# Kernel tuning notes

Hardware: AMD Instinct MI355X
Metric: run time of the kernel (lower is better)

## Reference

```python
import jax, jax.numpy as jnp
import numpy as np

B, N, IN_DIM, OUT_DIM, H = 8, 1024, 256, 256, 4
HD = OUT_DIM // H  # head_dim = 64
NEG = -1e9
EPS = 1e-5


def setup_inputs() -> dict:
    key = jax.random.key(0)
    ks = jax.random.split(key, 9)
    h = jax.random.normal(ks[0], (B, N, IN_DIM), dtype=jnp.float32)
    adj = jax.random.randint(ks[1], (N, N), 0, 2, dtype=jnp.int32)
    adj = adj.at[jnp.arange(N), jnp.arange(N)].set(1)  # self loops so no empty rows
    s = 1.0 / np.sqrt(IN_DIM)
    W = jax.random.uniform(ks[2], (H, IN_DIM, HD), jnp.float32, -s, s)
    sa = 1.0 / np.sqrt(2 * HD)
    a1 = jax.random.uniform(ks[3], (H, HD), jnp.float32, -sa, sa)
    a2 = jax.random.uniform(ks[4], (H, HD), jnp.float32, -sa, sa)
    sp = 1.0 / np.sqrt(OUT_DIM)
    proj_w = jax.random.uniform(ks[5], (OUT_DIM, OUT_DIM), jnp.float32, -sp, sp)
    proj_b = jax.random.uniform(ks[6], (OUT_DIM,), jnp.float32, -sp, sp)
    gamma = jnp.ones((OUT_DIM,), jnp.float32)
    beta = jnp.zeros((OUT_DIM,), jnp.float32)
    return {"h": h, "adj": adj, "W": W, "a1": a1, "a2": a2,
            "proj_w": proj_w, "proj_b": proj_b, "gamma": gamma, "beta": beta}


def reference(h, adj, W, a1, a2, proj_w, proj_b, gamma, beta):
    # Wh: [B,H,N,HD]
    Wh = jnp.einsum('bni,hid->bhnd', h, W)
    # Decompose a([Wh_i || Wh_j]) = a1.Wh_i + a2.Wh_j (same math as concat+linear)
    si = jnp.einsum('bhnd,hd->bhn', Wh, a1)  # [B,H,N]
    sj = jnp.einsum('bhnd,hd->bhn', Wh, a2)
    e = jax.nn.leaky_relu(si[:, :, :, None] + sj[:, :, None, :], 0.2)  # [B,H,N,N]
    mask = (adj == 0)  # [N,N]
    e = jnp.where(mask[None, None], NEG, e)
    alpha = jax.nn.softmax(e, axis=-1)
    out = jnp.einsum('bhnm,bhmd->bhnd', alpha, Wh)  # [B,H,N,HD]
    h_multi = out.transpose(0, 2, 1, 3).reshape(B, N, OUT_DIM)  # concat heads
    h_out = jnp.einsum('bnd,od->bno', h_multi, proj_w) + proj_b
    h_out = h_out + h  # residual (in_dim == out_dim)
    mu = jnp.mean(h_out, axis=-1, keepdims=True)
    var = jnp.mean(jnp.square(h_out - mu), axis=-1, keepdims=True)
    return (h_out - mu) * jax.lax.rsqrt(var + EPS) * gamma + beta
```

## Files before the change

### kernel.cpp

```cpp
#include <hip/hip_runtime.h>
#include <hip/hip_bf16.h>

#define NN 1024

typedef __attribute__((ext_vector_type(8))) short short8;
typedef __attribute__((ext_vector_type(4))) short short4e;
typedef __attribute__((ext_vector_type(4))) float floatx4;
typedef __attribute__((ext_vector_type(4))) int intx4;

static __device__ __forceinline__ short bfb(float x) {
    return (short)__bfloat16_as_ushort(__float2bfloat16(x));
}

__global__ __launch_bounds__(256) void prep_kernel(
    const float* __restrict__ W, const float* __restrict__ proj_w,
    const int* __restrict__ adj,
    __hip_bfloat16* __restrict__ WTb,
    __hip_bfloat16* __restrict__ pwb,
    unsigned* __restrict__ adjm)
{
    int blk = blockIdx.x, t = threadIdx.x;
    if (blk < 16) {
        int o = blk * 16 + (t >> 4);
        int hh = o >> 6, d = o & 63;
        #pragma unroll
        for (int kk = 0; kk < 16; ++kk) {
            int k = (t & 15) + 16 * kk;
            WTb[(size_t)o * 256 + k] = __float2bfloat16(W[((size_t)hh * 256 + k) * 64 + d]);
        }
    } else if (blk < 32) {
        size_t base = (size_t)(blk - 16) * 4096 + (size_t)t * 16;
        #pragma unroll
        for (int k = 0; k < 16; k += 4) {
            floatx4 v = *(const floatx4*)(proj_w + base + k);
            short4e tmp;
            #pragma unroll
            for (int j = 0; j < 4; ++j) tmp[j] = bfb(v[j]);
            *(short4e*)(pwb + base + k) = tmp;
        }
    } else {
        int n = (blk - 32) * 8 + (t >> 5);
        int wd = t & 31;
        const int* arow = adj + (size_t)n * NN + wd * 32;
        unsigned bits = 0;
        #pragma unroll
        for (int j4 = 0; j4 < 8; ++j4) {
            intx4 v = *(const intx4*)(arow + j4 * 4);
            #pragma unroll
            for (int j = 0; j < 4; ++j) if (v[j] != 0) bits |= (1u << (j4 * 4 + j));
        }
        adjm[(size_t)n * 32 + wd] = bits;
    }
}

__global__ __launch_bounds__(256) void wh_kernel(
    const float* __restrict__ h,
    const __hip_bfloat16* __restrict__ WTb,
    const float* __restrict__ a1, const float* __restrict__ a2,
    __hip_bfloat16* __restrict__ WhT,
    float* __restrict__ si, float* __restrict__ sj)
{
    int t = threadIdx.x;
    int w = t >> 6, l = t & 63;
    int rl = l & 15, q = l >> 4;
    int r0 = blockIdx.x * 16;
    int bb = r0 >> 10;
    int n0 = r0 & 1023;

    __shared__ float redsi[4][4][16];
    __shared__ float redsj[4][4][16];

    short8 af[8];
    const float* Arow = h + (size_t)(r0 + rl) * 256 + q * 8;
    #pragma unroll
    for (int k0 = 0; k0 < 8; ++k0) {
        floatx4 v0 = *(const floatx4*)(Arow + k0 * 32);
        floatx4 v1 = *(const floatx4*)(Arow + k0 * 32 + 4);
        short8 a;
        #pragma unroll
        for (int j = 0; j < 4; ++j) { a[j] = bfb(v0[j]); a[j + 4] = bfb(v1[j]); }
        af[k0] = a;
    }

    float a1v[4], a2v[4];
    #pragma unroll
    for (int j = 0; j < 4; ++j) {
        a1v[j] = a1[j * 64 + w * 16 + rl];
        a2v[j] = a2[j * 64 + w * 16 + rl];
    }

    short8 bcur[8];
    {
        const __hip_bfloat16* B0 = WTb + (size_t)(w * 16 + rl) * 256 + q * 8;
        #pragma unroll
        for (int k0 = 0; k0 < 8; ++k0) bcur[k0] = *(const short8*)(B0 + k0 * 32);
    }

    #pragma unroll
    for (int j = 0; j < 4; ++j) {
        short8 bnxt[8];
        if (j < 3) {
            const __hip_bfloat16* Bn = WTb + (size_t)((w + (j + 1) * 4) * 16 + rl) * 256 + q * 8;
            #pragma unroll
            for (int k0 = 0; k0 < 8; ++k0) bnxt[k0] = *(const short8*)(Bn + k0 * 32);
        }

        floatx4 acc = {0.f, 0.f, 0.f, 0.f};
        #pragma unroll
        for (int k0 = 0; k0 < 8; ++k0)
            acc = __builtin_amdgcn_mfma_f32_16x16x32_bf16(af[k0], bcur[k0], acc, 0, 0, 0);

        short4e tmp;
        #pragma unroll
        for (int i = 0; i < 4; ++i) tmp[i] = bfb(acc[i]);
        *(short4e*)(WhT + ((size_t)(bb * 4 + j) * 64 + w * 16 + rl) * NN + n0 + q * 4) = tmp;

        #pragma unroll
        for (int i = 0; i < 4; ++i) {
            float p1 = acc[i] * a1v[j];
            float p2 = acc[i] * a2v[j];
            #pragma unroll
            for (int off = 1; off < 16; off <<= 1) {
                p1 += __shfl_xor(p1, off, 64);
                p2 += __shfl_xor(p2, off, 64);
            }
            if (rl == 0) { redsi[w][j][q * 4 + i] = p1; redsj[w][j][q * 4 + i] = p2; }
        }

        #pragma unroll
        for (int z = 0; z < 8; ++z) bcur[z] = bnxt[z];
    }
    __syncthreads();

    if (w == 0) {
        int head = l >> 4, row = l & 15;
        float s = redsi[0][head][row] + redsi[1][head][row] + redsi[2][head][row] + redsi[3][head][row];
        si[(size_t)(bb * 4 + head) * NN + n0 + row] = s;
    } else if (w == 1) {
        int head = l >> 4, row = l & 15;
        float s = redsj[0][head][row] + redsj[1][head][row] + redsj[2][head][row] + redsj[3][head][row];
        sj[(size_t)(bb * 4 + head) * NN + n0 + row] = s;
    }
}

__global__ __launch_bounds__(256) void attn_proj_kernel(
    const unsigned* __restrict__ adjm,
    const __hip_bfloat16* __restrict__ WhT,
    const float* __restrict__ si, const float* __restrict__ sj,
    const __hip_bfloat16* __restrict__ pwb,
    const float* __restrict__ h,
    const float* __restrict__ proj_b, const float* __restrict__ gamma,
    const float* __restrict__ beta,
    float* __restrict__ out)
{
    int blk = blockIdx.x, t = threadIdx.x;
    int w = t >> 6, l = t & 63;
    int rl = l & 15, q = l >> 4;
    int b = blk >> 6, n0 = (blk & 63) * 16;
    int bh = b * 4 + w;
    int r0 = blk * 16;

    __shared__ __align__(16) __hip_bfloat16 p_lds[4][16 * 136];
    __shared__ __align__(16) __hip_bfloat16 hm_stage[16][264];
    __shared__ float rinvs[4][16];
    __shared__ float red[2][4][16];

    int r = l >> 2, cg = l & 3;
    float sii = si[(size_t)bh * NN + n0 + r];
    const float* sjr = sj + (size_t)bh * NN;
    const unsigned* amrow = adjm + (size_t)(n0 + r) * 32;

    __hip_bfloat16* pt = &p_lds[w][0];
    const __hip_bfloat16* Ab = pt + rl * 136 + q * 8;
    const __hip_bfloat16* Bbase = WhT + ((size_t)bh * 64 + rl) * NN + q * 8;

    float lsum = 0.f;
    floatx4 acc[4] = { {0,0,0,0}, {0,0,0,0}, {0,0,0,0}, {0,0,0,0} };

#define SCORE_BLOCK(ITX)                                                        \
    do {                                                                        \
        int mb_ = (ITX) * 128 + cg * 32;                                        \
        unsigned bits_ = amrow[mb_ >> 5];                                       \
        short8 pv_[4];                                                          \
        _Pragma("unroll")                                                       \
        for (int c4 = 0; c4 < 8; ++c4) {                                        \
            floatx4 s4_ = *(const floatx4*)(sjr + mb_ + c4 * 4);                \
            _Pragma("unroll")                                                   \
            for (int k = 0; k < 4; ++k) {                                       \
                float x_ = sii + s4_[k];                                        \
                x_ = x_ > 0.f ? x_ : 0.2f * x_;                                 \
                x_ = ((bits_ >> (c4 * 4 + k)) & 1u) ? x_ : -1e9f;               \
                float pv = __expf(x_);                                          \
                lsum += pv;                                                     \
                pv_[c4 >> 1][(c4 & 1) * 4 + k] = bfb(pv);                       \
            }                                                                   \
        }                                                                       \
        short8* dst_ = (short8*)(pt + r * 136 + cg * 32);                       \
        dst_[0] = pv_[0]; dst_[1] = pv_[1]; dst_[2] = pv_[2]; dst_[3] = pv_[3]; \
    } while (0)

    short8 bcur[16];
    #pragma unroll
    for (int ks = 0; ks < 4; ++ks)
        #pragma unroll
        for (int dt = 0; dt < 4; ++dt)
            bcur[ks * 4 + dt] = *(const short8*)(Bbase + (size_t)dt * 16 * NN + ks * 32);
    SCORE_BLOCK(0);

    #pragma unroll
    for (int it = 0; it < 8; ++it) {
        short8 bnxt[16];
        if (it < 7) {
            int m1 = (it + 1) * 128;
            #pragma unroll
            for (int ks = 0; ks < 4; ++ks)
                #pragma unroll
                for (int dt = 0; dt < 4; ++dt)
                    bnxt[ks * 4 + dt] = *(const short8*)(Bbase + (size_t)dt * 16 * NN + m1 + ks * 32);
        }
        #pragma unroll
        for (int ks = 0; ks < 4; ++ks) {
            short8 afr = *(const short8*)(Ab + ks * 32);
            #pragma unroll
            for (int dt = 0; dt < 4; ++dt)
                acc[dt] = __builtin_amdgcn_mfma_f32_16x16x32_bf16(afr, bcur[ks * 4 + dt], acc[dt], 0, 0, 0);
        }
        if (it < 7) {
            SCORE_BLOCK(it + 1);
            #pragma unroll
            for (int z = 0; z < 16; ++z) bcur[z] = bnxt[z];
        }
    }
#undef SCORE_BLOCK

    lsum += __shfl_xor(lsum, 1, 64);
    lsum += __shfl_xor(lsum, 2, 64);
    if (cg == 0) rinvs[w][r] = 1.f / lsum;
    float riv[4];
    #pragma unroll
    for (int i = 0; i < 4; ++i) riv[i] = rinvs[w][q * 4 + i];

    #pragma unroll
    for (int dt = 0; dt < 4; ++dt) {
        #pragma unroll
        for (int i = 0; i < 4; ++i)
            hm_stage[q * 4 + i][w * 64 + dt * 16 + rl] = __float2bfloat16(acc[dt][i] * riv[i]);
    }
    __syncthreads();

    short8 paf[8];
    const __hip_bfloat16* Arow2 = &hm_stage[rl][0] + q * 8;
    #pragma unroll
    for (int k0 = 0; k0 < 8; ++k0) paf[k0] = *(const short8*)(Arow2 + k0 * 32);

    floatx4 pacc[4];
    #pragma unroll
    for (int j = 0; j < 4; ++j) {
        int ct = w + j * 4;
        const __hip_bfloat16* Brow = pwb + (size_t)(ct * 16 + rl) * 256 + q * 8;
        floatx4 a = {0.f, 0.f, 0.f, 0.f};
        #pragma unroll
        for (int k0 = 0; k0 < 8; ++k0) {
            short8 bfr = *(const short8*)(Brow + k0 * 32);
            a = __builtin_amdgcn_mfma_f32_16x16x32_bf16(paf[k0], bfr, a, 0, 0, 0);
        }
        pacc[j] = a;
    }

    float ps[4] = {0.f, 0.f, 0.f, 0.f};
    #pragma unroll
    for (int j = 0; j < 4; ++j) {
        int col = (w + j * 4) * 16 + rl;
        float pb = proj_b[col];
        #pragma unroll
        for (int i = 0; i < 4; ++i) {
            float v = pacc[j][i] + pb + h[(size_t)(r0 + q * 4 + i) * 256 + col];
            pacc[j][i] = v;
            ps[i] += v;
        }
    }
    #pragma unroll
    for (int i = 0; i < 4; ++i) {
        float s = ps[i];
        #pragma unroll
        for (int off = 1; off < 16; off <<= 1) s += __shfl_xor(s, off, 64);
        ps[i] = s;
    }
    if (rl == 0) {
        for (int i = 0; i < 4; ++i) red[0][w][q * 4 + i] = ps[i];
    }
    __syncthreads();
    float mu[4];
    #pragma unroll
    for (int i = 0; i < 4; ++i) {
        int row = q * 4 + i;
        mu[i] = (red[0][0][row] + red[0][1][row] + red[0][2][row] + red[0][3][row]) * (1.f / 256.f);
    }

    float vs[4] = {0.f, 0.f, 0.f, 0.f};
    #pragma unroll
    for (int j = 0; j < 4; ++j) {
        #pragma unroll
        for (int i = 0; i < 4; ++i) { float cv = pacc[j][i] - mu[i]; vs[i] += cv * cv; }
    }
    #pragma unroll
    for (int i = 0; i < 4; ++i) {
        float s = vs[i];
        #pragma unroll
        for (int off = 1; off < 16; off <<= 1) s += __shfl_xor(s, off, 64);
        vs[i] = s;
    }
    if (rl == 0) {
        for (int i = 0; i < 4; ++i) red[1][w][q * 4 + i] = vs[i];
    }
    __syncthreads();
    float rs[4];
    #pragma unroll
    for (int i = 0; i < 4; ++i) {
        int row = q * 4 + i;
        float var = (red[1][0][row] + red[1][1][row] + red[1][2][row] + red[1][3][row]) * (1.f / 256.f);
        rs[i] = rsqrtf(var + 1e-5f);
    }
    #pragma unroll
    for (int j = 0; j < 4; ++j) {
        int col = (w + j * 4) * 16 + rl;
        float g = gamma[col], be = beta[col];
        #pragma unroll
        for (int i = 0; i < 4; ++i)
            out[(size_t)(r0 + q * 4 + i) * 256 + col] = (pacc[j][i] - mu[i]) * rs[i] * g + be;
    }
}

extern "C" void kernel_launch(void* const* d_in, const int* in_sizes, int n_in,
                              void* d_out, int out_size, void* d_ws, size_t ws_size,
                              hipStream_t stream) {
    const float* h      = (const float*)d_in[0];
    const int*   adj    = (const int*)d_in[1];
    const float* W      = (const float*)d_in[2];
    const float* a1     = (const float*)d_in[3];
    const float* a2     = (const float*)d_in[4];
    const float* proj_w = (const float*)d_in[5];
    const float* proj_b = (const float*)d_in[6];
    const float* gamma  = (const float*)d_in[7];
    const float* beta   = (const float*)d_in[8];
    float* out = (float*)d_out;

    char* ws = (char*)d_ws;
    __hip_bfloat16* WhT = (__hip_bfloat16*)ws;   ws += (size_t)32 * 64 * NN * 2;
    __hip_bfloat16* WTb = (__hip_bfloat16*)ws;   ws += 256 * 256 * 2;
    __hip_bfloat16* pwb = (__hip_bfloat16*)ws;   ws += 256 * 256 * 2;
    float* si = (float*)ws;                      ws += (size_t)32 * NN * 4;
    float* sj = (float*)ws;                      ws += (size_t)32 * NN * 4;
    unsigned* adjm = (unsigned*)ws;              ws += (size_t)NN * 32 * 4;

    prep_kernel<<<160, 256, 0, stream>>>(W, proj_w, adj, WTb, pwb, adjm);
    wh_kernel<<<512, 256, 0, stream>>>(h, WTb, a1, a2, WhT, si, sj);
    attn_proj_kernel<<<512, 256, 0, stream>>>(adjm, WhT, si, sj, pwb, h, proj_b, gamma, beta, out);
}
```

Baseline: 146.0 us.

## Split attention and projection kernels, stage B operands through LDS with coalesced loads

After: 125.2 us. 14.2% less time.

```diff
diff --git a/kernel.cpp b/kernel.cpp
--- a/kernel.cpp
+++ b/kernel.cpp
@@ -2,14 +2,24 @@
 #include <hip/hip_bf16.h>
 
 #define NN 1024
+#define LOG2E 1.44269504088896f
 
 typedef __attribute__((ext_vector_type(8))) short short8;
 typedef __attribute__((ext_vector_type(4))) short short4e;
 typedef __attribute__((ext_vector_type(4))) float floatx4;
 typedef __attribute__((ext_vector_type(4))) int intx4;
-
-static __device__ __forceinline__ short bfb(float x) {
-    return (short)__bfloat16_as_ushort(__float2bfloat16(x));
+typedef __attribute__((ext_vector_type(2))) int intx2;
+
+static __device__ __forceinline__ unsigned pk2(float f0, float f1) {
+    unsigned u0 = __float_as_uint(f0) + 0x8000u;
+    unsigned u1 = __float_as_uint(f1) + 0x8000u;
+    return __builtin_amdgcn_perm(u1, u0, 0x07060302u);
+}
+static __device__ __forceinline__ short8 pk8(floatx4 v0, floatx4 v1) {
+    union { intx4 i; short8 s; } u;
+    u.i[0] = (int)pk2(v0[0], v0[1]); u.i[1] = (int)pk2(v0[2], v0[3]);
+    u.i[2] = (int)pk2(v1[0], v1[1]); u.i[3] = (int)pk2(v1[2], v1[3]);
+    return u.s;
 }
 
 __global__ __launch_bounds__(256) void prep_kernel(
@@ -31,12 +41,10 @@
     } else if (blk < 32) {
         size_t base = (size_t)(blk - 16) * 4096 + (size_t)t * 16;
         #pragma unroll
-        for (int k = 0; k < 16; k += 4) {
-            floatx4 v = *(const floatx4*)(proj_w + base + k);
-            short4e tmp;
-            #pragma unroll
-            for (int j = 0; j < 4; ++j) tmp[j] = bfb(v[j]);
-            *(short4e*)(pwb + base + k) = tmp;
+        for (int k = 0; k < 16; k += 8) {
+            floatx4 v0 = *(const floatx4*)(proj_w + base + k);
+            floatx4 v1 = *(const floatx4*)(proj_w + base + k + 4);
+            *(short8*)(pwb + base + k) = pk8(v0, v1);
         }
     } else {
         int n = (blk - 32) * 8 + (t >> 5);
@@ -64,9 +72,9 @@
     int w = t >> 6, l = t & 63;
     int rl = l & 15, q = l >> 4;
     int r0 = blockIdx.x * 16;
-    int bb = r0 >> 10;
-    int n0 = r0 & 1023;
-
+    int bb = r0 >> 10, n0 = r0 & 1023;
+
+    __shared__ __align__(16) __hip_bfloat16 bst[4][16][264];
     __shared__ float redsi[4][4][16];
     __shared__ float redsj[4][4][16];
 
@@ -76,49 +84,43 @@
     for (int k0 = 0; k0 < 8; ++k0) {
         floatx4 v0 = *(const floatx4*)(Arow + k0 * 32);
         floatx4 v1 = *(const floatx4*)(Arow + k0 * 32 + 4);
-        short8 a;
-        #pragma unroll
-        for (int j = 0; j < 4; ++j) { a[j] = bfb(v0[j]); a[j + 4] = bfb(v1[j]); }
-        af[k0] = a;
-    }
-
-    float a1v[4], a2v[4];
-    #pragma unroll
-    for (int j = 0; j < 4; ++j) {
-        a1v[j] = a1[j * 64 + w * 16 + rl];
-        a2v[j] = a2[j * 64 + w * 16 + rl];
-    }
-
-    short8 bcur[8];
+        af[k0] = pk8(v0, v1);
+    }
+
+    short8 sreg[8], nreg[8];
     {
-        const __hip_bfloat16* B0 = WTb + (size_t)(w * 16 + rl) * 256 + q * 8;
-        #pragma unroll
-        for (int k0 = 0; k0 < 8; ++k0) bcur[k0] = *(const short8*)(B0 + k0 * 32);
-    }
-
-    #pragma unroll
-    for (int j = 0; j < 4; ++j) {
-        short8 bnxt[8];
+        const __hip_bfloat16* src = WTb + (size_t)w * 16 * 256;
+        #pragma unroll
+        for (int k = 0; k < 8; ++k) sreg[k] = *(const short8*)(src + k * 512 + l * 8);
+    }
+
+    #pragma unroll
+    for (int j = 0; j < 4; ++j) {
         if (j < 3) {
-            const __hip_bfloat16* Bn = WTb + (size_t)((w + (j + 1) * 4) * 16 + rl) * 256 + q * 8;
-            #pragma unroll
-            for (int k0 = 0; k0 < 8; ++k0) bnxt[k0] = *(const short8*)(Bn + k0 * 32);
-        }
-
+            const __hip_bfloat16* src = WTb + (size_t)(w + 4 * (j + 1)) * 16 * 256;
+            #pragma unroll
+            for (int k = 0; k < 8; ++k) nreg[k] = *(const short8*)(src + k * 512 + l * 8);
+        }
+        #pragma unroll
+        for (int k = 0; k < 8; ++k)
+            *(short8*)(&bst[w][k * 2 + (l >> 5)][(l & 31) * 8]) = sreg[k];
         floatx4 acc = {0.f, 0.f, 0.f, 0.f};
         #pragma unroll
-        for (int k0 = 0; k0 < 8; ++k0)
-            acc = __builtin_amdgcn_mfma_f32_16x16x32_bf16(af[k0], bcur[k0], acc, 0, 0, 0);
-
-        short4e tmp;
-        #pragma unroll
-        for (int i = 0; i < 4; ++i) tmp[i] = bfb(acc[i]);
-        *(short4e*)(WhT + ((size_t)(bb * 4 + j) * 64 + w * 16 + rl) * NN + n0 + q * 4) = tmp;
-
+        for (int k0 = 0; k0 < 8; ++k0) {
+            short8 bf = *(const short8*)(&bst[w][rl][q * 8 + k0 * 32]);
+            acc = __builtin_amdgcn_mfma_f32_16x16x32_bf16(af[k0], bf, acc, 0, 0, 0);
+        }
+
+        intx2 pr;
+        pr[0] = (int)pk2(acc[0], acc[1]);
+        pr[1] = (int)pk2(acc[2], acc[3]);
+        *(intx2*)(WhT + ((size_t)(bb * 4 + j) * 64 + w * 16 + rl) * NN + n0 + q * 4) = pr;
+
+        float av1 = a1[j * 64 + w * 16 + rl] * LOG2E;
+        float av2 = a2[j * 64 + w * 16 + rl] * LOG2E;
         #pragma unroll
         for (int i = 0; i < 4; ++i) {
-            float p1 = acc[i] * a1v[j];
-            float p2 = acc[i] * a2v[j];
+            float p1 = acc[i] * av1, p2 = acc[i] * av2;
             #pragma unroll
             for (int off = 1; off < 16; off <<= 1) {
                 p1 += __shfl_xor(p1, off, 64);
@@ -126,145 +128,169 @@
             }
             if (rl == 0) { redsi[w][j][q * 4 + i] = p1; redsj[w][j][q * 4 + i] = p2; }
         }
-
-        #pragma unroll
-        for (int z = 0; z < 8; ++z) bcur[z] = bnxt[z];
+        #pragma unroll
+        for (int z = 0; z < 8; ++z) sreg[z] = nreg[z];
     }
     __syncthreads();
 
-    if (w == 0) {
-        int head = l >> 4, row = l & 15;
-        float s = redsi[0][head][row] + redsi[1][head][row] + redsi[2][head][row] + redsi[3][head][row];
-        si[(size_t)(bb * 4 + head) * NN + n0 + row] = s;
-    } else if (w == 1) {
-        int head = l >> 4, row = l & 15;
-        float s = redsj[0][head][row] + redsj[1][head][row] + redsj[2][head][row] + redsj[3][head][row];
-        sj[(size_t)(bb * 4 + head) * NN + n0 + row] = s;
-    }
-}
-
-__global__ __launch_bounds__(256) void attn_proj_kernel(
+    if (t < 64) {
+        int head = t >> 4, row = t & 15;
+        si[(size_t)(bb * 4 + head) * NN + n0 + row] =
+            redsi[0][head][row] + redsi[1][head][row] + redsi[2][head][row] + redsi[3][head][row];
+    } else if (t < 128) {
+        int u = t - 64;
+        int head = u >> 4, row = u & 15;
+        sj[(size_t)(bb * 4 + head) * NN + n0 + row] =
+            redsj[0][head][row] + redsj[1][head][row] + redsj[2][head][row] + redsj[3][head][row];
+    }
+}
+
+__global__ __launch_bounds__(256) void attn_kernel(
     const unsigned* __restrict__ adjm,
     const __hip_bfloat16* __restrict__ WhT,
     const float* __restrict__ si, const float* __restrict__ sj,
+    __hip_bfloat16* __restrict__ hmb)
+{
+    int bx = blockIdx.x, t = threadIdx.x;
+    int w = t >> 6, l = t & 63;
+    int rl = l & 15, q = l >> 4;
+    int b = bx >> 6, n0 = (bx & 63) * 16;
+    int bh = b * 4 + w;
+
+    __shared__ __align__(16) __hip_bfloat16 bst[4][64][72];
+    __shared__ __align__(16) __hip_bfloat16 p_lds[4][16][72];
+    __shared__ float rinvs[4][16];
+
+    int r = l >> 2, cg = l & 3;
+    float sii = si[(size_t)bh * NN + n0 + r];
+    const float* sjr = sj + (size_t)bh * NN;
+    const unsigned* amrow = adjm + (size_t)(n0 + r) * 32;
+
+    float lsum = 0.f;
+    floatx4 acc[4] = { {0,0,0,0}, {0,0,0,0}, {0,0,0,0}, {0,0,0,0} };
+
+    const __hip_bfloat16* Bsrc = WhT + (size_t)bh * 64 * NN;
+
+    short8 sreg[8], nreg[8];
+    #pragma unroll
+    for (int k = 0; k < 8; ++k)
+        sreg[k] = *(const short8*)(Bsrc + (size_t)(k * 8 + (l >> 3)) * NN + (l & 7) * 8);
+
+    #pragma unroll
+    for (int it = 0; it < 16; ++it) {
+        int m0 = it * 64;
+        if (it < 15) {
+            int m1 = m0 + 64;
+            #pragma unroll
+            for (int k = 0; k < 8; ++k)
+                nreg[k] = *(const short8*)(Bsrc + (size_t)(k * 8 + (l >> 3)) * NN + m1 + (l & 7) * 8);
+        }
+        {
+            int mb = m0 + cg * 16;
+            unsigned bits = amrow[(m0 >> 5) + (cg >> 1)] >> ((cg & 1) * 16);
+            unsigned pkd[4];
+            #pragma unroll
+            for (int c4 = 0; c4 < 4; ++c4) {
+                floatx4 s4 = *(const floatx4*)(sjr + mb + c4 * 4);
+                float pv[4];
+                #pragma unroll
+                for (int k = 0; k < 4; ++k) {
+                    float x = sii + s4[k];
+                    x = fmaxf(x, 0.2f * x);
+                    x = ((bits >> (c4 * 4 + k)) & 1u) ? x : -1e9f;
+                    pv[k] = exp2f(x);
+                    lsum += pv[k];
+                }
+                pkd[c4] = 0;
+                pkd[c4] = (unsigned)pk2(pv[0], pv[1]) | 0u;
+                unsigned hi = pk2(pv[2], pv[3]);
+                intx2 two; two[0] = (int)pkd[c4]; two[1] = (int)hi;
+                *(intx2*)(&p_lds[w][r][cg * 16 + c4 * 4]) = two;
+            }
+        }
+        #pragma unroll
+        for (int k = 0; k < 8; ++k)
+            *(short8*)(&bst[w][k * 8 + (l >> 3)][(l & 7) * 8]) = sreg[k];
+        #pragma unroll
+        for (int ks = 0; ks < 2; ++ks) {
+            short8 afr = *(const short8*)(&p_lds[w][rl][q * 8 + ks * 32]);
+            #pragma unroll
+            for (int dt = 0; dt < 4; ++dt) {
+                short8 bfr = *(const short8*)(&bst[w][dt * 16 + rl][q * 8 + ks * 32]);
+                acc[dt] = __builtin_amdgcn_mfma_f32_16x16x32_bf16(afr, bfr, acc[dt], 0, 0, 0);
+            }
+        }
+        #pragma unroll
+        for (int z = 0; z < 8; ++z) sreg[z] = nreg[z];
+    }
+
+    lsum += __shfl_xor(lsum, 1, 64);
+    lsum += __shfl_xor(lsum, 2, 64);
+    if (cg == 0) rinvs[w][r] = 1.f / lsum;
+    float riv[4];
+    #pragma unroll
+    for (int i = 0; i < 4; ++i) riv[i] = rinvs[w][q * 4 + i];
+
+    #pragma unroll
+    for (int dt = 0; dt < 4; ++dt) {
+        #pragma unroll
+        for (int i = 0; i < 4; ++i) {
+            float v = acc[dt][i] * riv[i];
+            unsigned uv = (__float_as_uint(v) + 0x8000u) >> 16;
+            hmb[((size_t)(b * NN) + n0 + q * 4 + i) * 256 + w * 64 + dt * 16 + rl] =
+                __ushort_as_bfloat16((unsigned short)uv);
+        }
+    }
+}
+
+__global__ __launch_bounds__(256) void proj_ln_kernel(
+    const __hip_bfloat16* __restrict__ hmb,
+    const float* __restrict__ h,
     const __hip_bfloat16* __restrict__ pwb,
-    const float* __restrict__ h,
     const float* __restrict__ proj_b, const float* __restrict__ gamma,
     const float* __restrict__ beta,
     float* __restrict__ out)
 {
-    int blk = blockIdx.x, t = threadIdx.x;
+    int t = threadIdx.x;
     int w = t >> 6, l = t & 63;
     int rl = l & 15, q = l >> 4;
-    int b = blk >> 6, n0 = (blk & 63) * 16;
-    int bh = b * 4 + w;
-    int r0 = blk * 16;
-
-    __shared__ __align__(16) __hip_bfloat16 p_lds[4][16 * 136];
-    __shared__ __align__(16) __hip_bfloat16 hm_stage[16][264];
-    __shared__ float rinvs[4][16];
+    int r0 = blockIdx.x * 16;
+
+    __shared__ __align__(16) __hip_bfloat16 bst[4][16][264];
     __shared__ float red[2][4][16];
 
-    int r = l >> 2, cg = l & 3;
-    float sii = si[(size_t)bh * NN + n0 + r];
-    const float* sjr = sj + (size_t)bh * NN;
-    const unsigned* amrow = adjm + (size_t)(n0 + r) * 32;
-
-    __hip_bfloat16* pt = &p_lds[w][0];
-    const __hip_bfloat16* Ab = pt + rl * 136 + q * 8;
-    const __hip_bfloat16* Bbase = WhT + ((size_t)bh * 64 + rl) * NN + q * 8;
-
-    float lsum = 0.f;
-    floatx4 acc[4] = { {0,0,0,0}, {0,0,0,0}, {0,0,0,0}, {0,0,0,0} };
-
-#define SCORE_BLOCK(ITX)                                                        \
-    do {                                                                        \
-        int mb_ = (ITX) * 128 + cg * 32;                                        \
-        unsigned bits_ = amrow[mb_ >> 5];                                       \
-        short8 pv_[4];                                                          \
-        _Pragma("unroll")                                                       \
-        for (int c4 = 0; c4 < 8; ++c4) {                                        \
-            floatx4 s4_ = *(const floatx4*)(sjr + mb_ + c4 * 4);                \
-            _Pragma("unroll")                                                   \
-            for (int k = 0; k < 4; ++k) {                                       \
-                float x_ = sii + s4_[k];                                        \
-                x_ = x_ > 0.f ? x_ : 0.2f * x_;                                 \
-                x_ = ((bits_ >> (c4 * 4 + k)) & 1u) ? x_ : -1e9f;               \
-                float pv = __expf(x_);                                          \
-                lsum += pv;                                                     \
-                pv_[c4 >> 1][(c4 & 1) * 4 + k] = bfb(pv);                       \
-            }                                                                   \
-        }                                                                       \
-        short8* dst_ = (short8*)(pt + r * 136 + cg * 32);                       \
-        dst_[0] = pv_[0]; dst_[1] = pv_[1]; dst_[2] = pv_[2]; dst_[3] = pv_[3]; \
-    } while (0)
-
-    short8 bcur[16];
-    #pragma unroll
-    for (int ks = 0; ks < 4; ++ks)
-        #pragma unroll
-        for (int dt = 0; dt < 4; ++dt)
-            bcur[ks * 4 + dt] = *(const short8*)(Bbase + (size_t)dt * 16 * NN + ks * 32);
-    SCORE_BLOCK(0);
-
-    #pragma unroll
-    for (int it = 0; it < 8; ++it) {
-        short8 bnxt[16];
-        if (it < 7) {
-            int m1 = (it + 1) * 128;
-            #pragma unroll
-            for (int ks = 0; ks < 4; ++ks)
-                #pragma unroll
-                for (int dt = 0; dt < 4; ++dt)
-                    bnxt[ks * 4 + dt] = *(const short8*)(Bbase + (size_t)dt * 16 * NN + m1 + ks * 32);
-        }
-        #pragma unroll
-        for (int ks = 0; ks < 4; ++ks) {
-            short8 afr = *(const short8*)(Ab + ks * 32);
-            #pragma unroll
-            for (int dt = 0; dt < 4; ++dt)
-                acc[dt] = __builtin_amdgcn_mfma_f32_16x16x32_bf16(afr, bcur[ks * 4 + dt], acc[dt], 0, 0, 0);
-        }
-        if (it < 7) {
-            SCORE_BLOCK(it + 1);
-            #pragma unroll
-            for (int z = 0; z < 16; ++z) bcur[z] = bnxt[z];
-        }
-    }
-#undef SCORE_BLOCK
-
-    lsum += __shfl_xor(lsum, 1, 64);
-    lsum += __shfl_xor(lsum, 2, 64);
-    if (cg == 0) rinvs[w][r] = 1.f / lsum;
-    float riv[4];
-    #pragma unroll
-    for (int i = 0; i < 4; ++i) riv[i] = rinvs[w][q * 4 + i];
-
-    #pragma unroll
-    for (int dt = 0; dt < 4; ++dt) {
-        #pragma unroll
-        for (int i = 0; i < 4; ++i)
-            hm_stage[q * 4 + i][w * 64 + dt * 16 + rl] = __float2bfloat16(acc[dt][i] * riv[i]);
-    }
-    __syncthreads();
-
-    short8 paf[8];
-    const __hip_bfloat16* Arow2 = &hm_stage[rl][0] + q * 8;
-    #pragma unroll
-    for (int k0 = 0; k0 < 8; ++k0) paf[k0] = *(const short8*)(Arow2 + k0 * 32);
+    short8 af[8];
+    const __hip_bfloat16* Arow = hmb + (size_t)(r0 + rl) * 256 + q * 8;
+    #pragma unroll
+    for (int k0 = 0; k0 < 8; ++k0) af[k0] = *(const short8*)(Arow + k0 * 32);
+
+    short8 sreg[8], nreg[8];
+    {
+        const __hip_bfloat16* src = pwb + (size_t)w * 16 * 256;
+        #pragma unroll
+        for (int k = 0; k < 8; ++k) sreg[k] = *(const short8*)(src + k * 512 + l * 8);
+    }
 
     floatx4 pacc[4];
     #pragma unroll
     for (int j = 0; j < 4; ++j) {
-        int ct = w + j * 4;
-        const __hip_bfloat16* Brow = pwb + (size_t)(ct * 16 + rl) * 256 + q * 8;
+        if (j < 3) {
+            const __hip_bfloat16* src = pwb + (size_t)(w + 4 * (j + 1)) * 16 * 256;
+            #pragma unroll
+            for (int k = 0; k < 8; ++k) nreg[k] = *(const short8*)(src + k * 512 + l * 8);
+        }
+        #pragma unroll
+        for (int k = 0; k < 8; ++k)
+            *(short8*)(&bst[w][k * 2 + (l >> 5)][(l & 31) * 8]) = sreg[k];
         floatx4 a = {0.f, 0.f, 0.f, 0.f};
         #pragma unroll
         for (int k0 = 0; k0 < 8; ++k0) {
-            short8 bfr = *(const short8*)(Brow + k0 * 32);
-            a = __builtin_amdgcn_mfma_f32_16x16x32_bf16(paf[k0], bfr, a, 0, 0, 0);
+            short8 bf = *(const short8*)(&bst[w][rl][q * 8 + k0 * 32]);
+            a = __builtin_amdgcn_mfma_f32_16x16x32_bf16(af[k0], bf, a, 0, 0, 0);
         }
         pacc[j] = a;
+        #pragma unroll
+        for (int z = 0; z < 8; ++z) sreg[z] = nreg[z];
     }
 
     float ps[4] = {0.f, 0.f, 0.f, 0.f};
@@ -296,7 +322,6 @@
         int row = q * 4 + i;
         mu[i] = (red[0][0][row] + red[0][1][row] + red[0][2][row] + red[0][3][row]) * (1.f / 256.f);
     }
-
     float vs[4] = {0.f, 0.f, 0.f, 0.f};
     #pragma unroll
     for (int j = 0; j < 4; ++j) {
@@ -347,6 +372,7 @@
 
     char* ws = (char*)d_ws;
     __hip_bfloat16* WhT = (__hip_bfloat16*)ws;   ws += (size_t)32 * 64 * NN * 2;
+    __hip_bfloat16* hmb = (__hip_bfloat16*)ws;   ws += (size_t)8 * NN * 256 * 2;
     __hip_bfloat16* WTb = (__hip_bfloat16*)ws;   ws += 256 * 256 * 2;
     __hip_bfloat16* pwb = (__hip_bfloat16*)ws;   ws += 256 * 256 * 2;
     float* si = (float*)ws;                      ws += (size_t)32 * NN * 4;
@@ -355,5 +381,6 @@
 
     prep_kernel<<<160, 256, 0, stream>>>(W, proj_w, adj, WTb, pwb, adjm);
     wh_kernel<<<512, 256, 0, stream>>>(h, WTb, a1, a2, WhT, si, sj);
-    attn_proj_kernel<<<512, 256, 0, stream>>>(adjm, WhT, si, sj, pwb, h, proj_b, gamma, beta, out);
-}
+    attn_kernel<<<512, 256, 0, stream>>>(adjm, WhT, si, sj, hmb);
+    proj_ln_kernel<<<512, 256, 0, stream>>>(hmb, h, pwb, proj_b, gamma, beta, out);
+}
```
